# Optimization experiments

Hardware: AMD Instinct MI355X
Metric: run time of the kernel (lower is better)

Reference implementation:

```python
import jax, jax.numpy as jnp
import numpy as np

D_MODEL = 256
NHEAD = 4
K_MODE = 8


def setup_inputs() -> dict:
    key = jax.random.key(0)
    ks = jax.random.split(key, 12)
    bs, S = 2, 4096
    inp = {
        "q": jax.random.normal(ks[0], (bs, S, D_MODEL), jnp.float32),
        "k": jax.random.normal(ks[1], (bs, S, D_MODEL + K_MODE), jnp.float32),
        "v": jax.random.normal(ks[2], (bs, S, D_MODEL), jnp.float32),
        "mask": jax.random.randint(ks[3], (bs, S, S), 0, 2, jnp.int32),
        # nn.Linear params: W is [out, in], y = x @ W.T + b
        "Wq": jax.random.normal(ks[4], (D_MODEL, D_MODEL), jnp.float32) * 0.02,
        "bq": jnp.zeros((D_MODEL,), jnp.float32),
        "Wk": jax.random.normal(ks[5], (D_MODEL, D_MODEL + K_MODE), jnp.float32) * 0.02,
        "bk": jnp.zeros((D_MODEL,), jnp.float32),
        "Wv": jax.random.normal(ks[6], (D_MODEL, D_MODEL), jnp.float32) * 0.02,
        "bv": jnp.zeros((D_MODEL,), jnp.float32),
        "Wo": jax.random.normal(ks[7], (D_MODEL, NHEAD * D_MODEL), jnp.float32) * 0.02,
        "bo": jnp.zeros((D_MODEL,), jnp.float32),
    }
    return inp


def reference(q, k, v, mask, Wq, bq, Wk, bk, Wv, bv, Wo, bo):
    # Projections (nn.Linear: x @ W.T + b). In the original module the projected
    # q/k/v are repeat-broadcast identically across all nhead heads (d_k = d_model),
    # and the mask broadcasts across heads too (dropout disabled). Hence every head
    # computes the exact same attention output; we compute it once and tile the
    # concat, which is mathematically identical and avoids redundant HBM traffic.
    qh = jnp.einsum('bsd,ed->bse', q, Wq) + bq   # [bs, S, d]
    kh = jnp.einsum('bsd,ed->bse', k, Wk) + bk   # [bs, S, d]
    vh = jnp.einsum('bsd,ed->bse', v, Wv) + bv   # [bs, S, d]

    scale = 1.0 / jnp.sqrt(jnp.asarray(D_MODEL, qh.dtype))
    scores = jnp.einsum('bqd,bkd->bqk', qh, kh) * scale  # [bs, S, S]
    scores = jnp.where(mask == 0, jnp.asarray(-1e9, scores.dtype), scores)
    attn = jax.nn.softmax(scores, axis=-1)
    per_head = jnp.einsum('bqk,bkd->bqd', attn, vh)      # [bs, S, d]

    concat = jnp.tile(per_head, (1, 1, NHEAD))           # [bs, S, h*d]
    return jnp.einsum('bsf,df->bsd', concat, Wo) + bo
```

## Files before the change

### kernel.cpp

```cpp
#include <hip/hip_runtime.h>

typedef unsigned short u16;
typedef unsigned int u32;
typedef unsigned long long u64;
typedef __bf16 bf16x8 __attribute__((ext_vector_type(8)));
typedef float f32x4 __attribute__((ext_vector_type(4)));

#define S_LEN 4096
#define DM 256

__device__ __forceinline__ u16 f2b(float f) {
  u32 u = __builtin_bit_cast(u32, f);
  u = (u + 0x7FFFu + ((u >> 16) & 1u)) >> 16;
  return (u16)u;
}
__device__ __forceinline__ float b2f(u16 b) {
  return __builtin_bit_cast(float, (u32)b << 16);
}

__device__ __forceinline__ f32x4 mfma16(bf16x8 a, bf16x8 b, f32x4 c) {
  return __builtin_amdgcn_mfma_f32_16x16x32_bf16(a, b, c, 0, 0, 0);
}

__device__ __forceinline__ void gl_lds16(const u16* g, u16* l) {
  __builtin_amdgcn_global_load_lds(
      (const __attribute__((address_space(1))) u32*)g,
      (__attribute__((address_space(3))) u32*)l, 16, 0, 0);
}

template <int TIN_F32, int TOUT_F32, int BIAS_MODE>
__global__ __launch_bounds__(256, 2) void gemm_nt_kernel(
    const void* __restrict__ Ap, const void* __restrict__ Bp,
    void* __restrict__ Cp, const float* __restrict__ bias, float scale,
    int M, int N, int K, int lda, int ldb, int ldc,
    long sA, long sB, long sC) {
  __shared__ u16 As[64][72];
  __shared__ u16 Bs[64][72];
  const int tid = threadIdx.x;
  const int w = tid >> 6, ln = tid & 63, lg = ln >> 4, ll = ln & 15;
  const int m0 = blockIdx.x * 64, n0 = blockIdx.y * 64;
  const long zA = (long)blockIdx.z * sA, zB = (long)blockIdx.z * sB,
             zC = (long)blockIdx.z * sC;

  const f32x4 fzero = {0.f, 0.f, 0.f, 0.f};
  f32x4 acc[4];
#pragma unroll
  for (int i = 0; i < 4; ++i) acc[i] = fzero;

  const int srow = tid >> 2, scb = (tid & 3) * 16;
  const int nk = (K + 63) >> 6;
  for (int kc = 0; kc < nk; ++kc) {
    const int k0 = kc * 64;
    if (TIN_F32) {
      {
        const float* src = (const float*)Ap + zA + (size_t)(m0 + srow) * lda + k0 + scb;
        u16 t[16];
        if (k0 + 64 <= K) {
#pragma unroll
          for (int i = 0; i < 16; ++i) t[i] = f2b(src[i]);
        } else {
#pragma unroll
          for (int i = 0; i < 16; ++i) {
            int gk = k0 + scb + i;
            t[i] = (gk < K) ? f2b(src[i]) : (u16)0;
          }
        }
#pragma unroll
        for (int i = 0; i < 16; ++i) As[srow][scb + i] = t[i];
      }
      {
        const float* src = (const float*)Bp + zB + (size_t)(n0 + srow) * ldb + k0 + scb;
        u16 t[16];
        if (k0 + 64 <= K) {
#pragma unroll
          for (int i = 0; i < 16; ++i) t[i] = f2b(src[i]);
        } else {
#pragma unroll
          for (int i = 0; i < 16; ++i) {
            int gk = k0 + scb + i;
            t[i] = (gk < K) ? f2b(src[i]) : (u16)0;
          }
        }
#pragma unroll
        for (int i = 0; i < 16; ++i) Bs[srow][scb + i] = t[i];
      }
    } else {
      const u16* srcA = (const u16*)Ap + zA + (size_t)(m0 + srow) * lda + k0 + scb;
      *(bf16x8*)&As[srow][scb] = *(const bf16x8*)srcA;
      *(bf16x8*)&As[srow][scb + 8] = *(const bf16x8*)(srcA + 8);
      const u16* srcB = (const u16*)Bp + zB + (size_t)(n0 + srow) * ldb + k0 + scb;
      *(bf16x8*)&Bs[srow][scb] = *(const bf16x8*)srcB;
      *(bf16x8*)&Bs[srow][scb + 8] = *(const bf16x8*)(srcB + 8);
    }
    __syncthreads();
#pragma unroll
    for (int ks = 0; ks < 2; ++ks) {
      bf16x8 af = *(const bf16x8*)&As[w * 16 + ll][ks * 32 + lg * 8];
#pragma unroll
      for (int ct = 0; ct < 4; ++ct) {
        bf16x8 bfr = *(const bf16x8*)&Bs[ct * 16 + ll][ks * 32 + lg * 8];
        acc[ct] = mfma16(af, bfr, acc[ct]);
      }
    }
    __syncthreads();
  }

#pragma unroll
  for (int ct = 0; ct < 4; ++ct) {
#pragma unroll
    for (int j = 0; j < 4; ++j) {
      int row = m0 + w * 16 + lg * 4 + j;
      int col = n0 + ct * 16 + ll;
      float v = acc[ct][j];
      if (BIAS_MODE == 1) v += bias[col];
      if (BIAS_MODE == 2) v += bias[row];
      v *= scale;
      if (TOUT_F32)
        ((float*)Cp)[zC + (size_t)row * ldc + col] = v;
      else
        ((u16*)Cp)[zC + (size_t)row * ldc + col] = f2b(v);
    }
  }
}

__global__ void wos_kernel(const float* __restrict__ Wo, u16* __restrict__ WoS) {
  int d = blockIdx.x, e = threadIdx.x;
  const float* p = Wo + (size_t)d * 1024;
  WoS[(size_t)d * 256 + e] = f2b(p[e] + p[256 + e] + p[512 + e] + p[768 + e]);
}

__global__ __launch_bounds__(256) void bitpack_kernel(const int* __restrict__ mask,
                                                      u32* __restrict__ mb) {
  const int ln = threadIdx.x & 63;
  const int gw = (int)((blockIdx.x * 256 + threadIdx.x) >> 6);
  const int nw = gridDim.x * 4;
  u64* mb64 = (u64*)mb;
  for (int it = gw; it < 131072; it += nw) {
    const int* p = mask + (size_t)it * 256 + ln;
    int v0 = p[0], v1 = p[64], v2 = p[128], v3 = p[192];
    u64 b0 = __ballot(v0 != 0);
    u64 b1 = __ballot(v1 != 0);
    u64 b2 = __ballot(v2 != 0);
    u64 b3 = __ballot(v3 != 0);
    if (ln < 4) {
      u64 val = ln == 0 ? b0 : (ln == 1 ? b1 : (ln == 2 ? b2 : b3));
      mb64[(size_t)it * 4 + ln] = val;
    }
  }
}

__global__ __launch_bounds__(256, 2) void flash_kernel(
    const u16* __restrict__ qh, const u16* __restrict__ kh,
    const u16* __restrict__ vhT, const u32* __restrict__ mb,
    u16* __restrict__ Opart, float* __restrict__ Lpart) {
  __shared__ u16 kh_s[2][32 * 256];
  __shared__ u16 vs_s[2][256 * 32];
  __shared__ u16 p_s[4][32][40];

  const int tid = threadIdx.x;
  const int w = tid >> 6, ln = tid & 63, lg = ln >> 4, ll = ln & 15;
  const int q0 = blockIdx.x * 128;
  const int b = blockIdx.y;
  const int h = blockIdx.z;

  bf16x8 qf[2][8];
#pragma unroll
  for (int qg = 0; qg < 2; ++qg) {
    const u16* qp = qh + (size_t)(b * S_LEN + q0 + w * 32 + qg * 16 + ll) * DM + lg * 8;
#pragma unroll
    for (int ks = 0; ks < 8; ++ks) qf[qg][ks] = *(const bf16x8*)(qp + ks * 32);
  }

  const f32x4 fzero = {0.f, 0.f, 0.f, 0.f};
  f32x4 acc_o[2][16];
#pragma unroll
  for (int qg = 0; qg < 2; ++qg)
#pragma unroll
    for (int i = 0; i < 16; ++i) acc_o[qg][i] = fzero;
  float l_run[2][4] = {{0.f, 0.f, 0.f, 0.f}, {0.f, 0.f, 0.f, 0.f}};

  const u16* kbase = kh + (size_t)(b * S_LEN + h * 512) * DM;
  const u16* vbase = vhT + (size_t)b * DM * S_LEN + h * 512;
  const u32* mbase = mb + (size_t)(b * S_LEN + q0 + w * 32) * 128 + h * 16;

  auto stage = [&](int t, int buf) {
#pragma unroll
    for (int i = 0; i < 4; ++i) {
      int c = i * 256 + tid;
      int row = c >> 5, ccl = c & 31;
      int ccg = ccl ^ (row & 7);
      gl_lds16(kbase + (size_t)(t * 32 + row) * DM + ccg * 8,
               &kh_s[buf][(i * 256 + w * 64) * 8]);
    }
#pragma unroll
    for (int i = 0; i < 4; ++i) {
      int c = i * 256 + tid;
      int row = c >> 2, cc = c & 3;
      gl_lds16(vbase + (size_t)row * S_LEN + t * 32 + cc * 8,
               &vs_s[buf][(i * 256 + w * 64) * 8]);
    }
  };

  stage(0, 0);
  __syncthreads();

  int cur = 0;
  for (int t = 0; t < 16; ++t) {
    u32 mw[2][4];
#pragma unroll
    for (int qg = 0; qg < 2; ++qg)
#pragma unroll
      for (int j = 0; j < 4; ++j)
        mw[qg][j] = mbase[(size_t)(qg * 16 + lg * 4 + j) * 128 + t];

    if (t + 1 < 16) stage(t + 1, cur ^ 1);

    f32x4 accs[2][2];
    accs[0][0] = fzero;
    accs[0][1] = fzero;
    accs[1][0] = fzero;
    accs[1][1] = fzero;
#pragma unroll
    for (int ks = 0; ks < 8; ++ks) {
#pragma unroll
      for (int half = 0; half < 2; ++half) {
        int krow = half * 16 + ll;
        bf16x8 kf = *(const bf16x8*)&kh_s[cur][krow * 256 +
                                              (((ks * 4 + lg) ^ (krow & 7)) << 3)];
        accs[0][half] = mfma16(qf[0][ks], kf, accs[0][half]);
        accs[1][half] = mfma16(qf[1][ks], kf, accs[1][half]);
      }
    }

#pragma unroll
    for (int qg = 0; qg < 2; ++qg) {
#pragma unroll
      for (int j = 0; j < 4; ++j) {
        u32 m = mw[qg][j];
        float p0 = ((m >> ll) & 1u) ? __expf(accs[qg][0][j]) : 0.f;
        float p1 = ((m >> (16 + ll)) & 1u) ? __expf(accs[qg][1][j]) : 0.f;
        l_run[qg][j] += p0 + p1;
        int r = qg * 16 + lg * 4 + j;
        p_s[w][r][ll] = f2b(p0);
        p_s[w][r][16 + ll] = f2b(p1);
      }
    }
    bf16x8 pf0 = *(const bf16x8*)&p_s[w][ll][lg * 8];
    bf16x8 pf1 = *(const bf16x8*)&p_s[w][16 + ll][lg * 8];

#pragma unroll
    for (int dt = 0; dt < 16; ++dt) {
      int vrow = dt * 16 + ll;
      bf16x8 vf = *(const bf16x8*)&vs_s[cur][vrow * 32 + lg * 8];
      acc_o[0][dt] = mfma16(pf0, vf, acc_o[0][dt]);
      acc_o[1][dt] = mfma16(pf1, vf, acc_o[1][dt]);
    }
    __syncthreads();
    cur ^= 1;
  }

#pragma unroll
  for (int qg = 0; qg < 2; ++qg) {
#pragma unroll
    for (int j = 0; j < 4; ++j) {
      float l = l_run[qg][j];
      l += __shfl_xor(l, 1);
      l += __shfl_xor(l, 2);
      l += __shfl_xor(l, 4);
      l += __shfl_xor(l, 8);
      l_run[qg][j] = l;
    }
  }
  const size_t growb = (size_t)h * 8192 + (size_t)b * S_LEN + q0 + w * 32;
  if (ll == 0) {
#pragma unroll
    for (int qg = 0; qg < 2; ++qg)
#pragma unroll
      for (int j = 0; j < 4; ++j)
        Lpart[growb + qg * 16 + lg * 4 + j] = l_run[qg][j];
  }
#pragma unroll
  for (int qg = 0; qg < 2; ++qg)
#pragma unroll
    for (int dt = 0; dt < 16; ++dt)
#pragma unroll
      for (int j = 0; j < 4; ++j)
        Opart[(growb + qg * 16 + lg * 4 + j) * 256 + dt * 16 + ll] =
            f2b(acc_o[qg][dt][j]);
}

__global__ void combine_kernel(const u16* __restrict__ Opart,
                               const float* __restrict__ Lpart,
                               u16* __restrict__ ph) {
  const int r = blockIdx.x;
  const int d = threadIdx.x;
  float o = 0.f, l = 0.f;
#pragma unroll
  for (int s = 0; s < 8; ++s) {
    l += Lpart[(size_t)s * 8192 + r];
    o += b2f(Opart[((size_t)s * 8192 + r) * 256 + d]);
  }
  ph[(size_t)r * 256 + d] = f2b(o / l);
}

extern "C" void kernel_launch(void* const* d_in, const int* in_sizes, int n_in,
                              void* d_out, int out_size, void* d_ws, size_t ws_size,
                              hipStream_t stream) {
  const float* q = (const float*)d_in[0];
  const float* k = (const float*)d_in[1];
  const float* v = (const float*)d_in[2];
  const int* mask = (const int*)d_in[3];
  const float* Wq = (const float*)d_in[4];
  const float* bq = (const float*)d_in[5];
  const float* Wk = (const float*)d_in[6];
  const float* bk = (const float*)d_in[7];
  const float* Wv = (const float*)d_in[8];
  const float* bv = (const float*)d_in[9];
  const float* Wo = (const float*)d_in[10];
  const float* bo = (const float*)d_in[11];

  char* ws = (char*)d_ws;
  u16* qh = (u16*)(ws + 0);
  u16* kh = (u16*)(ws + 4194304);
  u16* vhT = (u16*)(ws + 8388608);
  u16* WoS = (u16*)(ws + 12582912);
  u32* mb = (u32*)(ws + 12713984);
  u16* Op = (u16*)(ws + 16908288);
  float* Lp = (float*)(ws + 50462720);

  dim3 blk(256);
  gemm_nt_kernel<1, 0, 1><<<dim3(128, 4, 1), blk, 0, stream>>>(
      q, Wq, qh, bq, 0.0625f, 8192, 256, 256, 256, 256, 256, 0, 0, 0);
  gemm_nt_kernel<1, 0, 1><<<dim3(128, 4, 1), blk, 0, stream>>>(
      k, Wk, kh, bk, 1.0f, 8192, 256, 264, 264, 264, 256, 0, 0, 0);
  gemm_nt_kernel<1, 0, 2><<<dim3(4, 64, 2), blk, 0, stream>>>(
      Wv, v, vhT, bv, 1.0f, 256, 4096, 256, 256, 256, 4096,
      0, (long)4096 * 256, (long)256 * 4096);
  wos_kernel<<<dim3(256), blk, 0, stream>>>(Wo, WoS);
  bitpack_kernel<<<dim3(2048), blk, 0, stream>>>(mask, mb);
  flash_kernel<<<dim3(32, 2, 8), blk, 0, stream>>>(qh, kh, vhT, mb, Op, Lp);
  combine_kernel<<<dim3(8192), blk, 0, stream>>>(Op, Lp, qh);
  gemm_nt_kernel<0, 1, 1><<<dim3(128, 4, 1), blk, 0, stream>>>(
      qh, WoS, d_out, bo, 1.0f, 8192, 256, 256, 256, 256, 256, 0, 0, 0);
}
```

Baseline: 133.4 us.

## Shrink flash tile to 16 query rows per wave, read V from global, remap grid

Each flash block now covers 64 query rows instead of 128, so each wave holds half the registers. Launch bounds rise to 4 blocks per SM and the grid grows to 1024 one-dimensional blocks. The remap places blocks with the same head/key split next to each other. V fragments are loaded straight from global memory rather than staged in LDS, which frees shared memory. The goals are higher occupancy and better L2 locality, at the cost of extra K staging per query and uncached global V loads inside the inner MFMA loop.

```diff
diff --git a/kernel.cpp b/kernel.cpp
--- a/kernel.cpp
+++ b/kernel.cpp
@@ -149,39 +149,36 @@
   }
 }
 
-__global__ __launch_bounds__(256, 2) void flash_kernel(
+__global__ __launch_bounds__(256, 4) void flash_kernel(
     const u16* __restrict__ qh, const u16* __restrict__ kh,
     const u16* __restrict__ vhT, const u32* __restrict__ mb,
     u16* __restrict__ Opart, float* __restrict__ Lpart) {
   __shared__ u16 kh_s[2][32 * 256];
-  __shared__ u16 vs_s[2][256 * 32];
-  __shared__ u16 p_s[4][32][40];
+  __shared__ u16 p_s[4][16][40];
 
   const int tid = threadIdx.x;
   const int w = tid >> 6, ln = tid & 63, lg = ln >> 4, ll = ln & 15;
-  const int q0 = blockIdx.x * 128;
-  const int b = blockIdx.y;
-  const int h = blockIdx.z;
-
-  bf16x8 qf[2][8];
-#pragma unroll
-  for (int qg = 0; qg < 2; ++qg) {
-    const u16* qp = qh + (size_t)(b * S_LEN + q0 + w * 32 + qg * 16 + ll) * DM + lg * 8;
-#pragma unroll
-    for (int ks = 0; ks < 8; ++ks) qf[qg][ks] = *(const bf16x8*)(qp + ks * 32);
+  const int wg = ((int)blockIdx.x & 7) * 128 + ((int)blockIdx.x >> 3);
+  const int q0 = (wg & 63) * 64;
+  const int b = (wg >> 6) & 1;
+  const int h = wg >> 7;
+
+  bf16x8 qf[8];
+  {
+    const u16* qp = qh + (size_t)(b * S_LEN + q0 + w * 16 + ll) * DM + lg * 8;
+#pragma unroll
+    for (int ks = 0; ks < 8; ++ks) qf[ks] = *(const bf16x8*)(qp + ks * 32);
   }
 
   const f32x4 fzero = {0.f, 0.f, 0.f, 0.f};
-  f32x4 acc_o[2][16];
-#pragma unroll
-  for (int qg = 0; qg < 2; ++qg)
-#pragma unroll
-    for (int i = 0; i < 16; ++i) acc_o[qg][i] = fzero;
-  float l_run[2][4] = {{0.f, 0.f, 0.f, 0.f}, {0.f, 0.f, 0.f, 0.f}};
+  f32x4 acc_o[16];
+#pragma unroll
+  for (int i = 0; i < 16; ++i) acc_o[i] = fzero;
+  float l_run[4] = {0.f, 0.f, 0.f, 0.f};
 
   const u16* kbase = kh + (size_t)(b * S_LEN + h * 512) * DM;
   const u16* vbase = vhT + (size_t)b * DM * S_LEN + h * 512;
-  const u32* mbase = mb + (size_t)(b * S_LEN + q0 + w * 32) * 128 + h * 16;
+  const u32* mbase = mb + (size_t)(b * S_LEN + q0 + w * 16) * 128 + h * 16;
 
   auto stage = [&](int t, int buf) {
 #pragma unroll
@@ -192,13 +189,6 @@
       gl_lds16(kbase + (size_t)(t * 32 + row) * DM + ccg * 8,
                &kh_s[buf][(i * 256 + w * 64) * 8]);
     }
-#pragma unroll
-    for (int i = 0; i < 4; ++i) {
-      int c = i * 256 + tid;
-      int row = c >> 2, cc = c & 3;
-      gl_lds16(vbase + (size_t)row * S_LEN + t * 32 + cc * 8,
-               &vs_s[buf][(i * 256 + w * 64) * 8]);
-    }
   };
 
   stage(0, 0);
@@ -206,20 +196,16 @@
 
   int cur = 0;
   for (int t = 0; t < 16; ++t) {
-    u32 mw[2][4];
-#pragma unroll
-    for (int qg = 0; qg < 2; ++qg)
-#pragma unroll
-      for (int j = 0; j < 4; ++j)
-        mw[qg][j] = mbase[(size_t)(qg * 16 + lg * 4 + j) * 128 + t];
+    u32 mw[4];
+#pragma unroll
+    for (int j = 0; j < 4; ++j)
+      mw[j] = mbase[(size_t)(lg * 4 + j) * 128 + t];
 
     if (t + 1 < 16) stage(t + 1, cur ^ 1);
 
-    f32x4 accs[2][2];
-    accs[0][0] = fzero;
-    accs[0][1] = fzero;
-    accs[1][0] = fzero;
-    accs[1][1] = fzero;
+    f32x4 accs[2];
+    accs[0] = fzero;
+    accs[1] = fzero;
 #pragma unroll
     for (int ks = 0; ks < 8; ++ks) {
 #pragma unroll
@@ -227,66 +213,51 @@
         int krow = half * 16 + ll;
         bf16x8 kf = *(const bf16x8*)&kh_s[cur][krow * 256 +
                                               (((ks * 4 + lg) ^ (krow & 7)) << 3)];
-        accs[0][half] = mfma16(qf[0][ks], kf, accs[0][half]);
-        accs[1][half] = mfma16(qf[1][ks], kf, accs[1][half]);
+        accs[half] = mfma16(qf[ks], kf, accs[half]);
       }
     }
 
 #pragma unroll
-    for (int qg = 0; qg < 2; ++qg) {
-#pragma unroll
-      for (int j = 0; j < 4; ++j) {
-        u32 m = mw[qg][j];
-        float p0 = ((m >> ll) & 1u) ? __expf(accs[qg][0][j]) : 0.f;
-        float p1 = ((m >> (16 + ll)) & 1u) ? __expf(accs[qg][1][j]) : 0.f;
-        l_run[qg][j] += p0 + p1;
-        int r = qg * 16 + lg * 4 + j;
-        p_s[w][r][ll] = f2b(p0);
-        p_s[w][r][16 + ll] = f2b(p1);
-      }
-    }
-    bf16x8 pf0 = *(const bf16x8*)&p_s[w][ll][lg * 8];
-    bf16x8 pf1 = *(const bf16x8*)&p_s[w][16 + ll][lg * 8];
+    for (int j = 0; j < 4; ++j) {
+      u32 m = mw[j];
+      float p0 = ((m >> ll) & 1u) ? __expf(accs[0][j]) : 0.f;
+      float p1 = ((m >> (16 + ll)) & 1u) ? __expf(accs[1][j]) : 0.f;
+      l_run[j] += p0 + p1;
+      int r = lg * 4 + j;
+      p_s[w][r][ll] = f2b(p0);
+      p_s[w][r][16 + ll] = f2b(p1);
+    }
+    bf16x8 pf = *(const bf16x8*)&p_s[w][ll][lg * 8];
 
 #pragma unroll
     for (int dt = 0; dt < 16; ++dt) {
-      int vrow = dt * 16 + ll;
-      bf16x8 vf = *(const bf16x8*)&vs_s[cur][vrow * 32 + lg * 8];
-      acc_o[0][dt] = mfma16(pf0, vf, acc_o[0][dt]);
-      acc_o[1][dt] = mfma16(pf1, vf, acc_o[1][dt]);
+      const u16* vp = vbase + (size_t)(dt * 16 + ll) * S_LEN + t * 32 + lg * 8;
+      bf16x8 vf = *(const bf16x8*)vp;
+      acc_o[dt] = mfma16(pf, vf, acc_o[dt]);
     }
     __syncthreads();
     cur ^= 1;
   }
 
 #pragma unroll
-  for (int qg = 0; qg < 2; ++qg) {
-#pragma unroll
-    for (int j = 0; j < 4; ++j) {
-      float l = l_run[qg][j];
-      l += __shfl_xor(l, 1);
-      l += __shfl_xor(l, 2);
-      l += __shfl_xor(l, 4);
-      l += __shfl_xor(l, 8);
-      l_run[qg][j] = l;
-    }
-  }
-  const size_t growb = (size_t)h * 8192 + (size_t)b * S_LEN + q0 + w * 32;
+  for (int j = 0; j < 4; ++j) {
+    float l = l_run[j];
+    l += __shfl_xor(l, 1);
+    l += __shfl_xor(l, 2);
+    l += __shfl_xor(l, 4);
+    l += __shfl_xor(l, 8);
+    l_run[j] = l;
+  }
+  const size_t growb = (size_t)h * 8192 + (size_t)b * S_LEN + q0 + w * 16;
   if (ll == 0) {
 #pragma unroll
-    for (int qg = 0; qg < 2; ++qg)
-#pragma unroll
-      for (int j = 0; j < 4; ++j)
-        Lpart[growb + qg * 16 + lg * 4 + j] = l_run[qg][j];
-  }
-#pragma unroll
-  for (int qg = 0; qg < 2; ++qg)
-#pragma unroll
-    for (int dt = 0; dt < 16; ++dt)
-#pragma unroll
-      for (int j = 0; j < 4; ++j)
-        Opart[(growb + qg * 16 + lg * 4 + j) * 256 + dt * 16 + ll] =
-            f2b(acc_o[qg][dt][j]);
+    for (int j = 0; j < 4; ++j) Lpart[growb + lg * 4 + j] = l_run[j];
+  }
+#pragma unroll
+  for (int dt = 0; dt < 16; ++dt)
+#pragma unroll
+    for (int j = 0; j < 4; ++j)
+      Opart[(growb + lg * 4 + j) * 256 + dt * 16 + ll] = f2b(acc_o[dt][j]);
 }
 
 __global__ void combine_kernel(const u16* __restrict__ Opart,
@@ -338,7 +309,7 @@
       0, (long)4096 * 256, (long)256 * 4096);
   wos_kernel<<<dim3(256), blk, 0, stream>>>(Wo, WoS);
   bitpack_kernel<<<dim3(2048), blk, 0, stream>>>(mask, mb);
-  flash_kernel<<<dim3(32, 2, 8), blk, 0, stream>>>(qh, kh, vhT, mb, Op, Lp);
+  flash_kernel<<<dim3(1024), blk, 0, stream>>>(qh, kh, vhT, mb, Op, Lp);
   combine_kernel<<<dim3(8192), blk, 0, stream>>>(Op, Lp, qh);
   gemm_nt_kernel<0, 1, 1><<<dim3(128, 4, 1), blk, 0, stream>>>(
       qh, WoS, d_out, bo, 1.0f, 8192, 256, 256, 256, 256, 256, 0, 0, 0);
```

Result: slower. 272.5 us (+104.3%).

## Compute transposed QK^T scores and pass P to PV MFMA via shuffles

Applied to the files above, without the earlier changes.

Swaps the MFMA operand order so each lane holds scores for a single query row across keys. The probabilities can then be packed to bf16 with v_cvt_pk_bf16_f32 and redistributed with cross-lane shuffles, which removes the LDS round-trip through p_s. Mask loading and the row-sum reduction become simpler, with one mask word per qg per lane. V tiles in LDS get an XOR swizzle to cut bank conflicts on the PV reads. The risk lies in the shuffle mapping's correctness and the extra shuffle instructions.

```diff
diff --git a/kernel.cpp b/kernel.cpp
--- a/kernel.cpp
+++ b/kernel.cpp
@@ -5,6 +5,7 @@
 typedef unsigned long long u64;
 typedef __bf16 bf16x8 __attribute__((ext_vector_type(8)));
 typedef float f32x4 __attribute__((ext_vector_type(4)));
+typedef u32 u32x4 __attribute__((ext_vector_type(4)));
 
 #define S_LEN 4096
 #define DM 256
@@ -155,7 +156,6 @@
     u16* __restrict__ Opart, float* __restrict__ Lpart) {
   __shared__ u16 kh_s[2][32 * 256];
   __shared__ u16 vs_s[2][256 * 32];
-  __shared__ u16 p_s[4][32][40];
 
   const int tid = threadIdx.x;
   const int w = tid >> 6, ln = tid & 63, lg = ln >> 4, ll = ln & 15;
@@ -177,7 +177,7 @@
   for (int qg = 0; qg < 2; ++qg)
 #pragma unroll
     for (int i = 0; i < 16; ++i) acc_o[qg][i] = fzero;
-  float l_run[2][4] = {{0.f, 0.f, 0.f, 0.f}, {0.f, 0.f, 0.f, 0.f}};
+  float l_run[2] = {0.f, 0.f};
 
   const u16* kbase = kh + (size_t)(b * S_LEN + h * 512) * DM;
   const u16* vbase = vhT + (size_t)b * DM * S_LEN + h * 512;
@@ -195,8 +195,9 @@
 #pragma unroll
     for (int i = 0; i < 4; ++i) {
       int c = i * 256 + tid;
-      int row = c >> 2, cc = c & 3;
-      gl_lds16(vbase + (size_t)row * S_LEN + t * 32 + cc * 8,
+      int row = c >> 2, ccl = c & 3;
+      int ccg = ccl ^ ((row >> 1) & 3);
+      gl_lds16(vbase + (size_t)row * S_LEN + t * 32 + ccg * 8,
                &vs_s[buf][(i * 256 + w * 64) * 8]);
     }
   };
@@ -206,12 +207,8 @@
 
   int cur = 0;
   for (int t = 0; t < 16; ++t) {
-    u32 mw[2][4];
-#pragma unroll
-    for (int qg = 0; qg < 2; ++qg)
-#pragma unroll
-      for (int j = 0; j < 4; ++j)
-        mw[qg][j] = mbase[(size_t)(qg * 16 + lg * 4 + j) * 128 + t];
+    u32 mw0 = mbase[(size_t)ll * 128 + t];
+    u32 mw1 = mbase[(size_t)(16 + ll) * 128 + t];
 
     if (t + 1 < 16) stage(t + 1, cur ^ 1);
 
@@ -227,57 +224,64 @@
         int krow = half * 16 + ll;
         bf16x8 kf = *(const bf16x8*)&kh_s[cur][krow * 256 +
                                               (((ks * 4 + lg) ^ (krow & 7)) << 3)];
-        accs[0][half] = mfma16(qf[0][ks], kf, accs[0][half]);
-        accs[1][half] = mfma16(qf[1][ks], kf, accs[1][half]);
+        accs[0][half] = mfma16(kf, qf[0][ks], accs[0][half]);
+        accs[1][half] = mfma16(kf, qf[1][ks], accs[1][half]);
       }
     }
 
+    bf16x8 pf[2];
 #pragma unroll
     for (int qg = 0; qg < 2; ++qg) {
-#pragma unroll
-      for (int j = 0; j < 4; ++j) {
-        u32 m = mw[qg][j];
-        float p0 = ((m >> ll) & 1u) ? __expf(accs[qg][0][j]) : 0.f;
-        float p1 = ((m >> (16 + ll)) & 1u) ? __expf(accs[qg][1][j]) : 0.f;
-        l_run[qg][j] += p0 + p1;
-        int r = qg * 16 + lg * 4 + j;
-        p_s[w][r][ll] = f2b(p0);
-        p_s[w][r][16 + ll] = f2b(p1);
-      }
-    }
-    bf16x8 pf0 = *(const bf16x8*)&p_s[w][ll][lg * 8];
-    bf16x8 pf1 = *(const bf16x8*)&p_s[w][16 + ll][lg * 8];
+      u32 m = qg ? mw1 : mw0;
+      float p[2][4];
+#pragma unroll
+      for (int half = 0; half < 2; ++half)
+#pragma unroll
+        for (int j = 0; j < 4; ++j) {
+          int bitpos = half * 16 + lg * 4 + j;
+          float pv = ((m >> bitpos) & 1u) ? __expf(accs[qg][half][j]) : 0.f;
+          p[half][j] = pv;
+          l_run[qg] += pv;
+        }
+      u32 c0, c1, c2, c3;
+      asm("v_cvt_pk_bf16_f32 %0, %1, %2" : "=v"(c0) : "v"(p[0][0]), "v"(p[0][1]));
+      asm("v_cvt_pk_bf16_f32 %0, %1, %2" : "=v"(c1) : "v"(p[0][2]), "v"(p[0][3]));
+      asm("v_cvt_pk_bf16_f32 %0, %1, %2" : "=v"(c2) : "v"(p[1][0]), "v"(p[1][1]));
+      asm("v_cvt_pk_bf16_f32 %0, %1, %2" : "=v"(c3) : "v"(p[1][2]), "v"(p[1][3]));
+      int sa = ll + ((lg & 1) << 5);
+      int sb = sa + 16;
+      u32 t0 = (u32)__shfl((int)c0, sa), t1 = (u32)__shfl((int)c1, sa);
+      u32 t2 = (u32)__shfl((int)c2, sa), t3 = (u32)__shfl((int)c3, sa);
+      u32 u0 = (u32)__shfl((int)c0, sb), u1 = (u32)__shfl((int)c1, sb);
+      u32 u2 = (u32)__shfl((int)c2, sb), u3 = (u32)__shfl((int)c3, sb);
+      bool hi = (lg & 2) != 0;
+      u32x4 pw;
+      pw.x = hi ? t2 : t0;
+      pw.y = hi ? t3 : t1;
+      pw.z = hi ? u2 : u0;
+      pw.w = hi ? u3 : u1;
+      pf[qg] = __builtin_bit_cast(bf16x8, pw);
+    }
 
 #pragma unroll
     for (int dt = 0; dt < 16; ++dt) {
       int vrow = dt * 16 + ll;
-      bf16x8 vf = *(const bf16x8*)&vs_s[cur][vrow * 32 + lg * 8];
-      acc_o[0][dt] = mfma16(pf0, vf, acc_o[0][dt]);
-      acc_o[1][dt] = mfma16(pf1, vf, acc_o[1][dt]);
+      bf16x8 vf = *(const bf16x8*)&vs_s[cur][vrow * 32 +
+                                            ((lg ^ ((vrow >> 1) & 3)) << 3)];
+      acc_o[0][dt] = mfma16(pf[0], vf, acc_o[0][dt]);
+      acc_o[1][dt] = mfma16(pf[1], vf, acc_o[1][dt]);
     }
     __syncthreads();
     cur ^= 1;
   }
 
+  const size_t growb = (size_t)h * 8192 + (size_t)b * S_LEN + q0 + w * 32;
 #pragma unroll
   for (int qg = 0; qg < 2; ++qg) {
-#pragma unroll
-    for (int j = 0; j < 4; ++j) {
-      float l = l_run[qg][j];
-      l += __shfl_xor(l, 1);
-      l += __shfl_xor(l, 2);
-      l += __shfl_xor(l, 4);
-      l += __shfl_xor(l, 8);
-      l_run[qg][j] = l;
-    }
-  }
-  const size_t growb = (size_t)h * 8192 + (size_t)b * S_LEN + q0 + w * 32;
-  if (ll == 0) {
-#pragma unroll
-    for (int qg = 0; qg < 2; ++qg)
-#pragma unroll
-      for (int j = 0; j < 4; ++j)
-        Lpart[growb + qg * 16 + lg * 4 + j] = l_run[qg][j];
+    float l = l_run[qg];
+    l += __shfl_xor(l, 16);
+    l += __shfl_xor(l, 32);
+    if (lg == 0) Lpart[growb + qg * 16 + ll] = l;
   }
 #pragma unroll
   for (int qg = 0; qg < 2; ++qg)
```

Result: slower. 140.0 us (+5.0%).
